# Kernel tuning notes

Hardware: AMD Instinct MI355X
Metric: run time of the kernel (lower is better)

Reference implementation:

```python
import jax, jax.numpy as jnp
import numpy as np

jax.config.update("jax_enable_x64", True)  # exact int64 fixed-point requantization

QMIN, QMAX = 0, 255  # 8-bit asymmetric activations


def _mul_m0_shift(acc, M0, shift):
    """gemmlowp-style fixed-point rescale: round((acc*M0)>>31) >> shift (rounding)."""
    prod = acc.astype(jnp.int64) * M0.astype(jnp.int64)
    nudge = jnp.where(prod >= 0, jnp.int64(1 << 30), jnp.int64(1 - (1 << 30)))
    hi = (prod + nudge) >> 31  # rounding-doubling high mul
    sh = shift.astype(jnp.int64)
    return (hi + (jnp.int64(1) << (sh - 1))) >> sh  # rounding right shift


def _requant(acc, M0, shift, z_out):
    return jnp.clip(_mul_m0_shift(acc, M0, shift) + z_out, QMIN, QMAX).astype(jnp.int32)


def _qconv(q, w, z_in, M0, shift, z_out, pad):
    # int8-style conv: subtract input zero-point, integer accumulate (exact in fp32
    # since |acc| < 2^24 by construction), then fixed-point requantize.
    xf = (q - z_in).astype(jnp.float32)
    acc = jax.lax.conv_general_dilated(
        xf, w, (1, 1), [(pad, pad), (pad, pad)],
        dimension_numbers=("NCHW", "OIHW", "NCHW"))
    return _requant(jnp.round(acc).astype(jnp.int64), M0, shift, z_out)


def _qbn(q, z_in, w, b, M0, shift, z_out):
    # fused quantized BN: per-channel integer affine + fixed-point requantize
    acc = (q.astype(jnp.int64) - z_in) * w.astype(jnp.int64)[None, :, None, None] \
          + b.astype(jnp.int64)[None, :, None, None]
    return _requant(acc, M0, shift, z_out)


def setup_inputs() -> dict:
    key = jax.random.key(0)
    ks = jax.random.split(key, 10)
    B, Cin, H, W = 32, 256, 56, 56
    width, Cout = 64, 256
    x = jax.random.randint(ks[0], (B, Cin, H, W), 0, 256, dtype=jnp.int32)
    w1 = jax.random.randint(ks[1], (width, Cin, 1, 1), -63, 64).astype(jnp.float32)
    w2 = jax.random.randint(ks[2], (width, width, 3, 3), -63, 64).astype(jnp.float32)
    w3 = jax.random.randint(ks[3], (Cout, width, 1, 1), -63, 64).astype(jnp.float32)
    bn1_w = jax.random.randint(ks[4], (width,), 100, 160).astype(jnp.float32)
    bn1_b = jax.random.randint(ks[5], (width,), -1000, 1000).astype(jnp.float32)
    bn2_w = jax.random.randint(ks[6], (width,), 100, 160).astype(jnp.float32)
    bn2_b = jax.random.randint(ks[7], (width,), -1000, 1000).astype(jnp.float32)
    bn3_w = jax.random.randint(ks[8], (Cout,), 100, 160).astype(jnp.float32)
    bn3_b = jax.random.randint(ks[9], (Cout,), -1000, 1000).astype(jnp.float32)
    conv_zin = jnp.array([128, 128, 128], jnp.int32)
    conv_m0 = jnp.array([1518500250] * 3, jnp.int32)
    conv_shift = jnp.array([9, 9, 9], jnp.int32)
    conv_zout = jnp.array([128, 128, 128], jnp.int32)
    bn_m0 = jnp.array([1073741824] * 3, jnp.int32)
    bn_shift = jnp.array([6, 6, 6], jnp.int32)
    bn_zout = jnp.array([128, 128, 128], jnp.int32)
    add_z = jnp.array([128, 128], jnp.int32)
    add_m0 = jnp.array([1073741824] * 2, jnp.int32)
    add_shift = jnp.array([1, 1], jnp.int32)
    add_zout = jnp.array(128, jnp.int32)
    return dict(x=x, w1=w1, w2=w2, w3=w3,
                bn1_w=bn1_w, bn1_b=bn1_b, bn2_w=bn2_w, bn2_b=bn2_b,
                bn3_w=bn3_w, bn3_b=bn3_b,
                conv_zin=conv_zin, conv_m0=conv_m0, conv_shift=conv_shift,
                conv_zout=conv_zout, bn_m0=bn_m0, bn_shift=bn_shift,
                bn_zout=bn_zout, add_z=add_z, add_m0=add_m0,
                add_shift=add_shift, add_zout=add_zout)


def reference(x, w1, w2, w3, bn1_w, bn1_b, bn2_w, bn2_b, bn3_w, bn3_b,
              conv_zin, conv_m0, conv_shift, conv_zout,
              bn_m0, bn_shift, bn_zout,
              add_z, add_m0, add_shift, add_zout):
    identity = x  # a_bit == target_bit -> rescale_matrix path skipped, conv_x = x
    out = _qconv(x, w1, conv_zin[0], conv_m0[0], conv_shift[0], conv_zout[0], 0)
    out = _qbn(out, conv_zout[0], bn1_w, bn1_b, bn_m0[0], bn_shift[0], bn_zout[0])
    out = _qconv(out, w2, conv_zin[1], conv_m0[1], conv_shift[1], conv_zout[1], 1)
    out = _qbn(out, conv_zout[1], bn2_w, bn2_b, bn_m0[1], bn_shift[1], bn_zout[1])
    out = _qconv(out, w3, conv_zin[2], conv_m0[2], conv_shift[2], conv_zout[2], 0)
    out = _qbn(out, conv_zout[2], bn3_w, bn3_b, bn_m0[2], bn_shift[2], bn_zout[2])
    # QuantizedAdd: rescale both branches to the output scale, add, clamp
    ra = _mul_m0_shift(identity.astype(jnp.int64) - add_z[0], add_m0[0], add_shift[0])
    rb = _mul_m0_shift(out.astype(jnp.int64) - add_z[1], add_m0[1], add_shift[1])
    return jnp.clip(ra + rb + add_zout, QMIN, QMAX).astype(jnp.int32)
```

## Files before the change

### kernel.cpp

```cpp
#include <hip/hip_runtime.h>


typedef int v4i __attribute__((ext_vector_type(4)));

#define BATCH 32
#define CIN 256
#define CMID 64
#define HW 3136
#define W56 56

#define T1_BYTES ((size_t)BATCH * HW * CMID)
#define WP_BYTES ((size_t)68 * 64 * 16)

__device__ __forceinline__ int requant_q(int acc, int M0, int shift, int zout) {
    long long prod = (long long)acc * (long long)M0;
    long long nudge = (prod >= 0) ? (1LL << 30) : (1LL - (1LL << 30));
    long long hi = (prod + nudge) >> 31;
    long long r = (hi + (1LL << (shift - 1))) >> shift;
    int v = (int)r + zout;
    return v < 0 ? 0 : (v > 255 ? 255 : v);
}

__device__ __forceinline__ long long mulshift_ll(long long v, int M0, int shift) {
    long long prod = v * (long long)M0;
    long long nudge = (prod >= 0) ? (1LL << 30) : (1LL - (1LL << 30));
    long long hi = (prod + nudge) >> 31;
    return (hi + (1LL << (shift - 1))) >> shift;
}

__device__ __forceinline__ v4i pack16f(const float* src, int stride) {
    v4i r;
#pragma unroll
    for (int d = 0; d < 4; ++d) {
        unsigned int u = 0;
#pragma unroll
        for (int by = 0; by < 4; ++by) {
            int v = (int)src[(d * 4 + by) * stride];
            u |= ((unsigned int)(v & 255)) << (8 * by);
        }
        r[d] = (int)u;
    }
    return r;
}

__global__ __launch_bounds__(256) void k_prep(
    const float* __restrict__ w1, const float* __restrict__ w2,
    const float* __restrict__ w3, v4i* __restrict__ wp)
{
    int id = blockIdx.x * 256 + threadIdx.x;
    int fid = id >> 6, lane = id & 63;
    if (fid >= 68) return;
    int col = lane & 15, ci0 = (lane >> 4) * 16;
    const float* src;
    int stride;
    if (fid < 16) {
        int wv = fid >> 2, ks = fid & 3;
        src = w1 + (size_t)(wv * 16 + col) * 256 + ks * 64 + ci0;
        stride = 1;
    } else if (fid < 52) {
        int i = fid - 16, wv = i / 9, t = i - wv * 9;
        src = w2 + ((size_t)(wv * 16 + col) * 64 + ci0) * 9 + t;
        stride = 9;
    } else {
        int s = fid - 52;
        src = w3 + (size_t)(s * 16 + col) * 64 + ci0;
        stride = 1;
    }
    wp[fid * 64 + lane] = pack16f(src, stride);
}

__global__ __launch_bounds__(256, 4) void k_conv1(
    const int* __restrict__ x, const v4i* __restrict__ wp1,
    const float* __restrict__ bn_w, const float* __restrict__ bn_b,
    const int* __restrict__ conv_zin, const int* __restrict__ conv_m0,
    const int* __restrict__ conv_shift, const int* __restrict__ conv_zout,
    const int* __restrict__ bn_m0, const int* __restrict__ bn_shift,
    const int* __restrict__ bn_zout, signed char* __restrict__ t1)
{
    __shared__ v4i sm[560];
    const int tid = threadIdx.x, lane = tid & 63, wv = tid >> 6;
    const int col = lane & 15, koff = lane >> 4;
    const int b = blockIdx.y;
    const int hw0 = blockIdx.x * 112;
    const int co0 = wv * 16;

    v4i a[4];
#pragma unroll
    for (int ks = 0; ks < 4; ++ks) a[ks] = wp1[(wv * 4 + ks) * 64 + lane];

    const int cg = tid & 7, q = tid >> 3;
    const bool act = q < 28;
    const int zin = conv_zin[0];
    const int* xbase = x + (size_t)b * CIN * HW + hw0 + 4 * q;

    v4i xa[8], xa2[8];
    if (act) {
#pragma unroll
        for (int j = 0; j < 8; ++j)
            xa[j] = *(const v4i*)(xbase + (size_t)(cg * 8 + j) * HW);
    }

    v4i acc[7];
#pragma unroll
    for (int i = 0; i < 7; ++i) acc[i] = (v4i){0, 0, 0, 0};

    unsigned long long* smu = (unsigned long long*)sm;
#pragma unroll
    for (int ks = 0; ks < 4; ++ks) {
        if (ks) __syncthreads();
        if (act) {
#pragma unroll
            for (int p = 0; p < 4; ++p) {
                unsigned int lo = 0, hi = 0;
#pragma unroll
                for (int j = 0; j < 4; ++j) {
                    lo |= ((unsigned int)((xa[j][p] - zin) & 255)) << (8 * j);
                    hi |= ((unsigned int)((xa[j + 4][p] - zin) & 255)) << (8 * j);
                }
                smu[(q * 4 + p) * 10 + cg] = ((unsigned long long)hi << 32) | lo;
            }
        }
        __syncthreads();
        if (ks < 3 && act) {
#pragma unroll
            for (int j = 0; j < 8; ++j)
                xa2[j] = *(const v4i*)(xbase + (size_t)((ks + 1) * 64 + cg * 8 + j) * HW);
        }
#pragma unroll
        for (int nt = 0; nt < 7; ++nt) {
            v4i bf = sm[(nt * 16 + col) * 5 + koff];
            acc[nt] = __builtin_amdgcn_mfma_i32_16x16x64_i8(a[ks], bf, acc[nt], 0, 0, 0);
        }
        if (ks < 3) {
#pragma unroll
            for (int j = 0; j < 8; ++j) xa[j] = xa2[j];
        }
    }

    const int cm0 = conv_m0[0], csh = conv_shift[0], czo = conv_zout[0];
    const int bm0 = bn_m0[0], bsh = bn_shift[0], bzo = bn_zout[0];
    const int zin2 = conv_zin[1];
    const int rowb = koff * 4;
    int bw[4], bb[4];
#pragma unroll
    for (int r = 0; r < 4; ++r) {
        bw[r] = (int)bn_w[co0 + rowb + r];
        bb[r] = (int)bn_b[co0 + rowb + r];
    }
#pragma unroll
    for (int nt = 0; nt < 7; ++nt) {
        int n = b * HW + hw0 + nt * 16 + col;
        unsigned int pkd = 0;
#pragma unroll
        for (int r = 0; r < 4; ++r) {
            int qv = requant_q(acc[nt][r], cm0, csh, czo);
            int a2 = (qv - czo) * bw[r] + bb[r];
            int q2 = requant_q(a2, bm0, bsh, bzo);
            pkd |= ((unsigned int)((q2 - zin2) & 255)) << (8 * r);
        }
        *(unsigned int*)(t1 + (size_t)n * 64 + co0 + rowb) = pkd;
    }
}

__global__ __launch_bounds__(256) void k_conv2(
    const signed char* __restrict__ t1, const v4i* __restrict__ wp2,
    const float* __restrict__ bn_w, const float* __restrict__ bn_b,
    const int* __restrict__ conv_zin, const int* __restrict__ conv_m0,
    const int* __restrict__ conv_shift, const int* __restrict__ conv_zout,
    const int* __restrict__ bn_m0, const int* __restrict__ bn_shift,
    const int* __restrict__ bn_zout, signed char* __restrict__ t2)
{
    __shared__ v4i sm[1680];
    const int tid = threadIdx.x, lane = tid & 63, wv = tid >> 6;
    const int col = lane & 15, koff = lane >> 4;
    const int b = blockIdx.y;
    const int r0 = blockIdx.x * 4;
    const int co0 = wv * 16;

    v4i a[9];
#pragma unroll
    for (int t = 0; t < 9; ++t) a[t] = wp2[(wv * 9 + t) * 64 + lane];

    const v4i* t1v = (const v4i*)t1;
#pragma unroll
    for (int k = 0; k < 6; ++k) {
        int idx = tid + k * 256;
        if (idx < 1344) {
            int pixl = idx >> 2, part = idx & 3;
            int lrow = pixl / W56, gw = pixl - lrow * W56;
            int grow = r0 - 1 + lrow;
            v4i v = (v4i){0, 0, 0, 0};
            if ((unsigned)grow < 56u)
                v = t1v[((size_t)b * HW + grow * W56 + gw) * 4 + part];
            sm[pixl * 5 + part] = v;
        }
    }
    __syncthreads();

    int orow[14], wc[14];
#pragma unroll
    for (int nt = 0; nt < 14; ++nt) {
        int pix = nt * 16 + col;
        orow[nt] = pix / W56;
        wc[nt] = pix - orow[nt] * W56;
    }

    v4i acc[14];
#pragma unroll
    for (int i = 0; i < 14; ++i) acc[i] = (v4i){0, 0, 0, 0};

#pragma unroll
    for (int kh = 0; kh < 3; ++kh) {
#pragma unroll
        for (int kw = 0; kw < 3; ++kw) {
            v4i af = a[kh * 3 + kw];
#pragma unroll
            for (int nt = 0; nt < 14; ++nt) {
                int sr = orow[nt] + kh;
                int sw = wc[nt] + kw - 1;
                bool valid = (unsigned)sw < 56u;
                v4i bf = sm[(sr * W56 + (valid ? sw : 0)) * 5 + koff];
                if (!valid) { bf[0] = 0; bf[1] = 0; bf[2] = 0; bf[3] = 0; }
                acc[nt] = __builtin_amdgcn_mfma_i32_16x16x64_i8(af, bf, acc[nt], 0, 0, 0);
            }
        }
    }

    const int cm0 = conv_m0[1], csh = conv_shift[1], czo = conv_zout[1];
    const int bm0 = bn_m0[1], bsh = bn_shift[1], bzo = bn_zout[1];
    const int zin3 = conv_zin[2];
    const int rowb = koff * 4;
    int bw[4], bb[4];
#pragma unroll
    for (int r = 0; r < 4; ++r) {
        bw[r] = (int)bn_w[co0 + rowb + r];
        bb[r] = (int)bn_b[co0 + rowb + r];
    }
#pragma unroll
    for (int nt = 0; nt < 14; ++nt) {
        int pix = nt * 16 + col;
        int n = b * HW + r0 * W56 + pix;
        unsigned int pkd = 0;
#pragma unroll
        for (int r = 0; r < 4; ++r) {
            int qv = requant_q(acc[nt][r], cm0, csh, czo);
            int a2 = (qv - czo) * bw[r] + bb[r];
            int q2 = requant_q(a2, bm0, bsh, bzo);
            pkd |= ((unsigned int)((q2 - zin3) & 255)) << (8 * r);
        }
        *(unsigned int*)(t2 + (size_t)n * 64 + co0 + rowb) = pkd;
    }
}

__global__ __launch_bounds__(256, 4) void k_conv3(
    const signed char* __restrict__ t2, const v4i* __restrict__ wp3,
    const float* __restrict__ bn_w, const float* __restrict__ bn_b,
    const int* __restrict__ x,
    const int* __restrict__ conv_m0, const int* __restrict__ conv_shift,
    const int* __restrict__ conv_zout,
    const int* __restrict__ bn_m0, const int* __restrict__ bn_shift,
    const int* __restrict__ bn_zout,
    const int* __restrict__ add_z, const int* __restrict__ add_m0,
    const int* __restrict__ add_shift, const int* __restrict__ add_zout,
    int* __restrict__ out)
{
    __shared__ v4i sm[640];
    const int tid = threadIdx.x, lane = tid & 63, wv = tid >> 6;
    const int col = lane & 15, koff = lane >> 4;
    const int nbase = blockIdx.x * 128;
    const int co0 = blockIdx.y * 64 + wv * 16;
    const int rowb = koff * 4;

    v4i a = wp3[(blockIdx.y * 4 + wv) * 64 + lane];

    int nn[8], pb[8], phw[8];
#pragma unroll
    for (int nt = 0; nt < 8; ++nt) {
        nn[nt] = nbase + nt * 16 + col;
        pb[nt] = nn[nt] / HW;
        phw[nt] = nn[nt] - pb[nt] * HW;
    }
    int xv[8][4];
#pragma unroll
    for (int nt = 0; nt < 8; ++nt)
#pragma unroll
        for (int r = 0; r < 4; ++r)
            xv[nt][r] = x[((size_t)pb[nt] * CIN + co0 + rowb + r) * HW + phw[nt]];

    const v4i* t2v = (const v4i*)t2;
#pragma unroll
    for (int k = 0; k < 2; ++k) {
        int idx = tid + k * 256;
        int pixl = idx >> 2, part = idx & 3;
        sm[pixl * 5 + part] = t2v[(size_t)(nbase + pixl) * 4 + part];
    }
    __syncthreads();

    v4i acc[8];
#pragma unroll
    for (int i = 0; i < 8; ++i) acc[i] = (v4i){0, 0, 0, 0};
#pragma unroll
    for (int nt = 0; nt < 8; ++nt) {
        v4i bf = sm[(nt * 16 + col) * 5 + koff];
        acc[nt] = __builtin_amdgcn_mfma_i32_16x16x64_i8(a, bf, acc[nt], 0, 0, 0);
    }

    const int cm0 = conv_m0[2], csh = conv_shift[2], czo = conv_zout[2];
    const int bm0 = bn_m0[2], bsh = bn_shift[2], bzo = bn_zout[2];
    const int az0 = add_z[0], az1 = add_z[1];
    const int am0 = add_m0[0], am1 = add_m0[1];
    const int ash0 = add_shift[0], ash1 = add_shift[1];
    const int azout = add_zout[0];
    int bw[4], bb[4];
#pragma unroll
    for (int r = 0; r < 4; ++r) {
        bw[r] = (int)bn_w[co0 + rowb + r];
        bb[r] = (int)bn_b[co0 + rowb + r];
    }
#pragma unroll
    for (int nt = 0; nt < 8; ++nt) {
#pragma unroll
        for (int r = 0; r < 4; ++r) {
            int qv = requant_q(acc[nt][r], cm0, csh, czo);
            int a2 = (qv - czo) * bw[r] + bb[r];
            int q2 = requant_q(a2, bm0, bsh, bzo);
            long long ra = mulshift_ll((long long)(xv[nt][r] - az0), am0, ash0);
            long long rb = mulshift_ll((long long)(q2 - az1), am1, ash1);
            int res = (int)(ra + rb) + azout;
            res = res < 0 ? 0 : (res > 255 ? 255 : res);
            out[((size_t)pb[nt] * CIN + co0 + rowb + r) * HW + phw[nt]] = res;
        }
    }
}

extern "C" void kernel_launch(void* const* d_in, const int* in_sizes, int n_in,
                              void* d_out, int out_size, void* d_ws, size_t ws_size,
                              hipStream_t stream) {
    const int* x = (const int*)d_in[0];
    const float* w1 = (const float*)d_in[1];
    const float* w2 = (const float*)d_in[2];
    const float* w3 = (const float*)d_in[3];
    const float* bn1_w = (const float*)d_in[4];
    const float* bn1_b = (const float*)d_in[5];
    const float* bn2_w = (const float*)d_in[6];
    const float* bn2_b = (const float*)d_in[7];
    const float* bn3_w = (const float*)d_in[8];
    const float* bn3_b = (const float*)d_in[9];
    const int* conv_zin = (const int*)d_in[10];
    const int* conv_m0 = (const int*)d_in[11];
    const int* conv_shift = (const int*)d_in[12];
    const int* conv_zout = (const int*)d_in[13];
    const int* bn_m0 = (const int*)d_in[14];
    const int* bn_shift = (const int*)d_in[15];
    const int* bn_zout = (const int*)d_in[16];
    const int* add_z = (const int*)d_in[17];
    const int* add_m0 = (const int*)d_in[18];
    const int* add_shift = (const int*)d_in[19];
    const int* add_zout = (const int*)d_in[20];

    v4i* wp = (v4i*)d_ws;
    signed char* t1 = (signed char*)d_ws + WP_BYTES;
    signed char* t2 = t1 + T1_BYTES;

    const v4i* wp1 = wp;
    const v4i* wp2 = wp + 16 * 64;
    const v4i* wp3 = wp + 52 * 64;

    k_prep<<<dim3(17), dim3(256), 0, stream>>>(w1, w2, w3, wp);
    k_conv1<<<dim3(28, 32), dim3(256), 0, stream>>>(x, wp1, bn1_w, bn1_b,
        conv_zin, conv_m0, conv_shift, conv_zout, bn_m0, bn_shift, bn_zout, t1);
    k_conv2<<<dim3(14, 32), dim3(256), 0, stream>>>(t1, wp2, bn2_w, bn2_b,
        conv_zin, conv_m0, conv_shift, conv_zout, bn_m0, bn_shift, bn_zout, t2);
    k_conv3<<<dim3(784, 4), dim3(256), 0, stream>>>(t2, wp3, bn3_w, bn3_b,
        x, conv_m0, conv_shift, conv_zout, bn_m0, bn_shift, bn_zout,
        add_z, add_m0, add_shift, add_zout, (int*)d_out);
}
```

Measured before the change: 276.4 us.

## Fold requant shifts into one, add LUTs for residual add, pad conv2 halo

Merges the two rounding shifts of the fixed-point requantize into a single add and shift with precomputed per-sign constants. In conv3, the two add-branch rescales are replaced by 256-entry shared-memory lookup tables built per block, since both inputs are 8-bit values. In conv2, the shared tile gets zeroed left and right halo columns so the inner MFMA loop drops its boundary checks and index math, and launch bounds are raised to 4 blocks per CU. Merging the shifts assumes the nudged product's low bits combine exactly like the two separate rounding steps, and the LUT assumes x lies in 0..255.

```diff
diff --git a/kernel.cpp b/kernel.cpp
--- a/kernel.cpp
+++ b/kernel.cpp
@@ -12,20 +12,12 @@
 #define T1_BYTES ((size_t)BATCH * HW * CMID)
 #define WP_BYTES ((size_t)68 * 64 * 16)
 
-__device__ __forceinline__ int requant_q(int acc, int M0, int shift, int zout) {
+__device__ __forceinline__ int requant_f(int acc, int M0, long long pAdd,
+                                         long long nAdd, int tSh, int zout) {
     long long prod = (long long)acc * (long long)M0;
-    long long nudge = (prod >= 0) ? (1LL << 30) : (1LL - (1LL << 30));
-    long long hi = (prod + nudge) >> 31;
-    long long r = (hi + (1LL << (shift - 1))) >> shift;
-    int v = (int)r + zout;
+    long long add = (prod >= 0) ? pAdd : nAdd;
+    int v = (int)((prod + add) >> tSh) + zout;
     return v < 0 ? 0 : (v > 255 ? 255 : v);
-}
-
-__device__ __forceinline__ long long mulshift_ll(long long v, int M0, int shift) {
-    long long prod = v * (long long)M0;
-    long long nudge = (prod >= 0) ? (1LL << 30) : (1LL - (1LL << 30));
-    long long hi = (prod + nudge) >> 31;
-    return (hi + (1LL << (shift - 1))) >> shift;
 }
 
 __device__ __forceinline__ v4i pack16f(const float* src, int stride) {
@@ -139,6 +131,11 @@
 
     const int cm0 = conv_m0[0], csh = conv_shift[0], czo = conv_zout[0];
     const int bm0 = bn_m0[0], bsh = bn_shift[0], bzo = bn_zout[0];
+    const long long cP = (1LL << 30) + (1LL << (30 + csh));
+    const long long cN = (1LL - (1LL << 30)) + (1LL << (30 + csh));
+    const long long bP = (1LL << 30) + (1LL << (30 + bsh));
+    const long long bN = (1LL - (1LL << 30)) + (1LL << (30 + bsh));
+    const int cT = 31 + csh, bT = 31 + bsh;
     const int zin2 = conv_zin[1];
     const int rowb = koff * 4;
     int bw[4], bb[4];
@@ -153,16 +150,16 @@
         unsigned int pkd = 0;
 #pragma unroll
         for (int r = 0; r < 4; ++r) {
-            int qv = requant_q(acc[nt][r], cm0, csh, czo);
+            int qv = requant_f(acc[nt][r], cm0, cP, cN, cT, czo);
             int a2 = (qv - czo) * bw[r] + bb[r];
-            int q2 = requant_q(a2, bm0, bsh, bzo);
+            int q2 = requant_f(a2, bm0, bP, bN, bT, bzo);
             pkd |= ((unsigned int)((q2 - zin2) & 255)) << (8 * r);
         }
         *(unsigned int*)(t1 + (size_t)n * 64 + co0 + rowb) = pkd;
     }
 }
 
-__global__ __launch_bounds__(256) void k_conv2(
+__global__ __launch_bounds__(256, 4) void k_conv2(
     const signed char* __restrict__ t1, const v4i* __restrict__ wp2,
     const float* __restrict__ bn_w, const float* __restrict__ bn_b,
     const int* __restrict__ conv_zin, const int* __restrict__ conv_m0,
@@ -170,7 +167,7 @@
     const int* __restrict__ bn_m0, const int* __restrict__ bn_shift,
     const int* __restrict__ bn_zout, signed char* __restrict__ t2)
 {
-    __shared__ v4i sm[1680];
+    __shared__ v4i sm[1740];
     const int tid = threadIdx.x, lane = tid & 63, wv = tid >> 6;
     const int col = lane & 15, koff = lane >> 4;
     const int b = blockIdx.y;
@@ -192,17 +189,22 @@
             v4i v = (v4i){0, 0, 0, 0};
             if ((unsigned)grow < 56u)
                 v = t1v[((size_t)b * HW + grow * W56 + gw) * 4 + part];
-            sm[pixl * 5 + part] = v;
-        }
+            sm[(lrow * 58 + gw + 1) * 5 + part] = v;
+        }
+    }
+    if (tid < 48) {
+        int e = tid >> 2, part = tid & 3;
+        int row = e >> 1, side = e & 1;
+        sm[(row * 58 + side * 57) * 5 + part] = (v4i){0, 0, 0, 0};
     }
     __syncthreads();
 
-    int orow[14], wc[14];
+    int basep[14];
 #pragma unroll
     for (int nt = 0; nt < 14; ++nt) {
         int pix = nt * 16 + col;
-        orow[nt] = pix / W56;
-        wc[nt] = pix - orow[nt] * W56;
+        int orow = pix / W56, wc = pix - orow * W56;
+        basep[nt] = (orow * 58 + wc) * 5 + koff;
     }
 
     v4i acc[14];
@@ -214,13 +216,10 @@
 #pragma unroll
         for (int kw = 0; kw < 3; ++kw) {
             v4i af = a[kh * 3 + kw];
+            const int toff = (kh * 58 + kw) * 5;
 #pragma unroll
             for (int nt = 0; nt < 14; ++nt) {
-                int sr = orow[nt] + kh;
-                int sw = wc[nt] + kw - 1;
-                bool valid = (unsigned)sw < 56u;
-                v4i bf = sm[(sr * W56 + (valid ? sw : 0)) * 5 + koff];
-                if (!valid) { bf[0] = 0; bf[1] = 0; bf[2] = 0; bf[3] = 0; }
+                v4i bf = sm[basep[nt] + toff];
                 acc[nt] = __builtin_amdgcn_mfma_i32_16x16x64_i8(af, bf, acc[nt], 0, 0, 0);
             }
         }
@@ -228,6 +227,11 @@
 
     const int cm0 = conv_m0[1], csh = conv_shift[1], czo = conv_zout[1];
     const int bm0 = bn_m0[1], bsh = bn_shift[1], bzo = bn_zout[1];
+    const long long cP = (1LL << 30) + (1LL << (30 + csh));
+    const long long cN = (1LL - (1LL << 30)) + (1LL << (30 + csh));
+    const long long bP = (1LL << 30) + (1LL << (30 + bsh));
+    const long long bN = (1LL - (1LL << 30)) + (1LL << (30 + bsh));
+    const int cT = 31 + csh, bT = 31 + bsh;
     const int zin3 = conv_zin[2];
     const int rowb = koff * 4;
     int bw[4], bb[4];
@@ -243,9 +247,9 @@
         unsigned int pkd = 0;
 #pragma unroll
         for (int r = 0; r < 4; ++r) {
-            int qv = requant_q(acc[nt][r], cm0, csh, czo);
+            int qv = requant_f(acc[nt][r], cm0, cP, cN, cT, czo);
             int a2 = (qv - czo) * bw[r] + bb[r];
-            int q2 = requant_q(a2, bm0, bsh, bzo);
+            int q2 = requant_f(a2, bm0, bP, bN, bT, bzo);
             pkd |= ((unsigned int)((q2 - zin3) & 255)) << (8 * r);
         }
         *(unsigned int*)(t2 + (size_t)n * 64 + co0 + rowb) = pkd;
@@ -265,6 +269,7 @@
     int* __restrict__ out)
 {
     __shared__ v4i sm[640];
+    __shared__ int lutA[256], lutB[256];
     const int tid = threadIdx.x, lane = tid & 63, wv = tid >> 6;
     const int col = lane & 15, koff = lane >> 4;
     const int nbase = blockIdx.x * 128;
@@ -273,6 +278,21 @@
 
     v4i a = wp3[(blockIdx.y * 4 + wv) * 64 + lane];
 
+    {
+        const int az0 = add_z[0], az1 = add_z[1];
+        const int am0 = add_m0[0], am1 = add_m0[1];
+        const int ash0 = add_shift[0], ash1 = add_shift[1];
+        const int azout = add_zout[0];
+        long long pA = (long long)(tid - az0) * am0;
+        long long pB = (long long)(tid - az1) * am1;
+        long long P0 = (1LL << 30) + (1LL << (30 + ash0));
+        long long N0 = (1LL - (1LL << 30)) + (1LL << (30 + ash0));
+        long long P1 = (1LL << 30) + (1LL << (30 + ash1));
+        long long N1 = (1LL - (1LL << 30)) + (1LL << (30 + ash1));
+        lutA[tid] = (int)((pA + (pA >= 0 ? P0 : N0)) >> (31 + ash0));
+        lutB[tid] = (int)((pB + (pB >= 0 ? P1 : N1)) >> (31 + ash1)) + azout;
+    }
+
     int nn[8], pb[8], phw[8];
 #pragma unroll
     for (int nt = 0; nt < 8; ++nt) {
@@ -307,10 +327,11 @@
 
     const int cm0 = conv_m0[2], csh = conv_shift[2], czo = conv_zout[2];
     const int bm0 = bn_m0[2], bsh = bn_shift[2], bzo = bn_zout[2];
-    const int az0 = add_z[0], az1 = add_z[1];
-    const int am0 = add_m0[0], am1 = add_m0[1];
-    const int ash0 = add_shift[0], ash1 = add_shift[1];
-    const int azout = add_zout[0];
+    const long long cP = (1LL << 30) + (1LL << (30 + csh));
+    const long long cN = (1LL - (1LL << 30)) + (1LL << (30 + csh));
+    const long long bP = (1LL << 30) + (1LL << (30 + bsh));
+    const long long bN = (1LL - (1LL << 30)) + (1LL << (30 + bsh));
+    const int cT = 31 + csh, bT = 31 + bsh;
     int bw[4], bb[4];
 #pragma unroll
     for (int r = 0; r < 4; ++r) {
@@ -321,12 +342,10 @@
     for (int nt = 0; nt < 8; ++nt) {
 #pragma unroll
         for (int r = 0; r < 4; ++r) {
-            int qv = requant_q(acc[nt][r], cm0, csh, czo);
+            int qv = requant_f(acc[nt][r], cm0, cP, cN, cT, czo);
             int a2 = (qv - czo) * bw[r] + bb[r];
-            int q2 = requant_q(a2, bm0, bsh, bzo);
-            long long ra = mulshift_ll((long long)(xv[nt][r] - az0), am0, ash0);
-            long long rb = mulshift_ll((long long)(q2 - az1), am1, ash1);
-            int res = (int)(ra + rb) + azout;
+            int q2 = requant_f(a2, bm0, bP, bN, bT, bzo);
+            int res = lutA[xv[nt][r]] + lutB[q2];
             res = res < 0 ? 0 : (res > 255 ? 255 : res);
             out[((size_t)pb[nt] * CIN + co0 + rowb + r) * HW + phw[nt]] = res;
         }
```

After: 283.7 us. +2.7%, slower.
